# Kernel tuning notes

Measured on AMD Instinct MI355X. Metric: run time of the kernel, lower is better.

## Reference

```python
import jax, jax.numpy as jnp
import numpy as np

B, T, N, DIN, HID, EMB, K, HOR, ODIM = 64, 12, 883, 1, 64, 10, 2, 12, 1


def setup_inputs() -> dict:
    key = jax.random.key(0)
    ks = jax.random.split(key, 12)
    s = 0.1  # keep gate pre-activations sane
    return dict(
        source=jax.random.normal(ks[0], (B, T, N, DIN), jnp.float32),
        node_emb=jax.random.normal(ks[1], (N, EMB), jnp.float32),
        w0_g=jax.random.normal(ks[2], (EMB, K, DIN + HID, 2 * HID), jnp.float32) * s,
        b0_g=jax.random.normal(ks[3], (EMB, 2 * HID), jnp.float32) * s,
        w0_c=jax.random.normal(ks[4], (EMB, K, DIN + HID, HID), jnp.float32) * s,
        b0_c=jax.random.normal(ks[5], (EMB, HID), jnp.float32) * s,
        w1_g=jax.random.normal(ks[6], (EMB, K, 2 * HID, 2 * HID), jnp.float32) * s,
        b1_g=jax.random.normal(ks[7], (EMB, 2 * HID), jnp.float32) * s,
        w1_c=jax.random.normal(ks[8], (EMB, K, 2 * HID, HID), jnp.float32) * s,
        b1_c=jax.random.normal(ks[9], (EMB, HID), jnp.float32) * s,
        conv_w=jax.random.normal(ks[10], (HOR * ODIM, 1, 1, HID), jnp.float32) * s,
        conv_b=jax.random.normal(ks[11], (HOR * ODIM,), jnp.float32) * s,
    )


def _supports(E):
    # adaptive adjacency: softmax(relu(E E^T)) row-wise, Chebyshev set [I, A, ...]
    A = jax.nn.softmax(jax.nn.relu(E @ E.T), axis=1)
    sup = [jnp.eye(E.shape[0], dtype=A.dtype), A]
    for _ in range(2, K):
        sup.append(2.0 * (A @ sup[-1]) - sup[-2])
    return jnp.stack(sup)  # [K, N, N]


def _gconv(x, E, sup, wpool, bpool):
    # x: [B,N,Cin] -> [B,N,Cout]; node-specific weights pooled from embeddings
    w = jnp.einsum('nd,dkio->nkio', E, wpool)          # [N,K,Cin,Cout]
    b = E @ bpool                                      # [N,Cout]
    xg = jnp.einsum('knm,bmc->bnkc', sup, x)           # [B,N,K,Cin]
    return jnp.einsum('bnki,nkio->bno', xg, w) + b


def _cell(x, h, E, sup, wg, bg, wc, bc):
    zr = jax.nn.sigmoid(_gconv(jnp.concatenate([x, h], -1), E, sup, wg, bg))
    z, r = jnp.split(zr, 2, axis=-1)
    hc = jnp.tanh(_gconv(jnp.concatenate([x, z * h], -1), E, sup, wc, bc))
    return r * h + (1.0 - r) * hc


def reference(source, node_emb, w0_g, b0_g, w0_c, b0_c, w1_g, b1_g, w1_c, b1_c, conv_w, conv_b):
    sup = _supports(node_emb)
    cur = jnp.transpose(source, (1, 0, 2, 3))  # [T,B,N,C]
    for wg, bg, wc, bc in ((w0_g, b0_g, w0_c, b0_c), (w1_g, b1_g, w1_c, b1_c)):
        h0 = jnp.zeros((source.shape[0], N, HID), source.dtype)

        def step(h, xt, wg=wg, bg=bg, wc=wc, bc=bc):
            hn = _cell(xt, h, node_emb, sup, wg, bg, wc, bc)
            return hn, hn

        _, cur = jax.lax.scan(step, h0, cur)  # [T,B,N,HID]
    last = cur[-1]  # [B,N,HID]
    # Conv2d(1, HOR*ODIM, kernel=(1,HID)) over [B,1,N,HID] == contraction over HID
    out = jnp.einsum('bnh,oh->bon', last, conv_w[:, 0, 0, :]) + conv_b[None, :, None]
    out = out.reshape(-1, HOR, ODIM, N).transpose(0, 1, 3, 2)  # [B,HOR,N,ODIM]
    return out
```

## Files before the change

### kernel.cpp

```cpp
#include <hip/hip_runtime.h>
#include <cstddef>

#define NN 883
#define BB 64
#define TT 12
#define EMB 10
#define KPAD 896

typedef short short8 __attribute__((ext_vector_type(8)));
typedef _Float16 half8 __attribute__((ext_vector_type(8)));
typedef float f32x4 __attribute__((ext_vector_type(4)));

__device__ __forceinline__ void split_f16(float v, _Float16* hp, _Float16* lp) {
  _Float16 h = (_Float16)v;
  *hp = h;
  *lp = (_Float16)(v - (float)h);
}

__global__ __launch_bounds__(256) void adj_kernel(const float* __restrict__ E,
                                                  _Float16* __restrict__ Ah,
                                                  _Float16* __restrict__ Al) {
  const int n = blockIdx.x;
  const int tid = threadIdx.x;
  __shared__ float sE[EMB];
  __shared__ float sred[256];
  if (tid < EMB) sE[tid] = E[n * EMB + tid];
  __syncthreads();
  float d[4];
  float lmax = 0.0f;
#pragma unroll
  for (int q = 0; q < 4; ++q) {
    int m = tid + q * 256;
    d[q] = 0.0f;
    if (m < NN) {
      float s = 0.0f;
#pragma unroll
      for (int e = 0; e < EMB; ++e) s += sE[e] * E[m * EMB + e];
      d[q] = fmaxf(s, 0.0f);
      lmax = fmaxf(lmax, d[q]);
    }
  }
  sred[tid] = lmax;
  __syncthreads();
  for (int s = 128; s > 0; s >>= 1) {
    if (tid < s) sred[tid] = fmaxf(sred[tid], sred[tid + s]);
    __syncthreads();
  }
  const float mx = sred[0];
  __syncthreads();
  float lsum = 0.0f;
#pragma unroll
  for (int q = 0; q < 4; ++q) {
    int m = tid + q * 256;
    if (m < NN) {
      d[q] = expf(d[q] - mx);
      lsum += d[q];
    }
  }
  sred[tid] = lsum;
  __syncthreads();
  for (int s = 128; s > 0; s >>= 1) {
    if (tid < s) sred[tid] += sred[tid + s];
    __syncthreads();
  }
  const float inv = 1.0f / sred[0];
#pragma unroll
  for (int q = 0; q < 4; ++q) {
    int m = tid + q * 256;
    if (m < KPAD) {
      float v = (m < NN) ? d[q] * inv : 0.0f;
      split_f16(v, &Ah[(size_t)n * KPAD + m], &Al[(size_t)n * KPAD + m]);
    }
  }
}

__global__ __launch_bounds__(256) void mfma_gemm3(const _Float16* __restrict__ Ah,
                                                  const _Float16* __restrict__ Al,
                                                  const _Float16* __restrict__ Xh,
                                                  const _Float16* __restrict__ Xl,
                                                  _Float16* __restrict__ Gh,
                                                  _Float16* __restrict__ Gl, int L) {
  __shared__ _Float16 sA[2][128][40];
  __shared__ _Float16 sX[2][4][128][8];
  const int tid = threadIdx.x;
  const int lane = tid & 63;
  const int wid = tid >> 6;
  const int wm = (wid >> 1) * 64, wn = (wid & 1) * 64;
  const int bm = blockIdx.y * 128;
  const int bl = blockIdx.x * 128;
  const int l15 = lane & 15, l4 = lane >> 4;

  f32x4 acc[4][4] = {};

  const int xlp = (tid & 63) * 2;
  const int xko = tid >> 6;

  for (int k0 = 0; k0 < KPAD; k0 += 32) {
    __syncthreads();
#pragma unroll
    for (int p = 0; p < 2; ++p) {
      int i = tid + p * 256;
      int m = i >> 2, k8 = (i & 3) * 8;
      *(half8*)&sA[0][m][k8] = *(const half8*)&Ah[(size_t)(bm + m) * KPAD + k0 + k8];
      *(half8*)&sA[1][m][k8] = *(const half8*)&Al[(size_t)(bm + m) * KPAD + k0 + k8];
    }
    {
      int gl = bl + xlp;
      int kb = k0 + xko * 8;
#pragma unroll
      for (int buf = 0; buf < 2; ++buf) {
        const _Float16* Xp = buf ? Xl : Xh;
        unsigned int v[8];
#pragma unroll
        for (int j = 0; j < 8; ++j)
          v[j] = *(const unsigned int*)&Xp[(size_t)(kb + j) * L + gl];
        short8 lo, hi;
#pragma unroll
        for (int j = 0; j < 8; ++j) {
          lo[j] = (short)(v[j] & 0xFFFFu);
          hi[j] = (short)(v[j] >> 16);
        }
        *(short8*)&sX[buf][xko][xlp][0] = lo;
        *(short8*)&sX[buf][xko][xlp + 1][0] = hi;
      }
    }
    __syncthreads();
    half8 afh[4], afl[4], bfh[4], bfl[4];
#pragma unroll
    for (int mi = 0; mi < 4; ++mi) {
      afh[mi] = *(half8*)&sA[0][wm + mi * 16 + l15][l4 * 8];
      afl[mi] = *(half8*)&sA[1][wm + mi * 16 + l15][l4 * 8];
    }
#pragma unroll
    for (int ni = 0; ni < 4; ++ni) {
      bfh[ni] = *(half8*)&sX[0][l4][wn + ni * 16 + l15][0];
      bfl[ni] = *(half8*)&sX[1][l4][wn + ni * 16 + l15][0];
    }
#pragma unroll
    for (int mi = 0; mi < 4; ++mi)
#pragma unroll
      for (int ni = 0; ni < 4; ++ni) {
        acc[mi][ni] = __builtin_amdgcn_mfma_f32_16x16x32_f16(afh[mi], bfh[ni],
                                                             acc[mi][ni], 0, 0, 0);
        acc[mi][ni] = __builtin_amdgcn_mfma_f32_16x16x32_f16(afh[mi], bfl[ni],
                                                             acc[mi][ni], 0, 0, 0);
        acc[mi][ni] = __builtin_amdgcn_mfma_f32_16x16x32_f16(afl[mi], bfh[ni],
                                                             acc[mi][ni], 0, 0, 0);
      }
  }
#pragma unroll
  for (int mi = 0; mi < 4; ++mi) {
    int row0 = bm + wm + mi * 16 + l4 * 4;
#pragma unroll
    for (int ni = 0; ni < 4; ++ni) {
      int col = bl + wn + ni * 16 + l15;
#pragma unroll
      for (int r = 0; r < 4; ++r) {
        int row = row0 + r;
        if (row < NN)
          split_f16(acc[mi][ni][r], &Gh[(size_t)row * L + col],
                    &Gl[(size_t)row * L + col]);
      }
    }
  }
}

__global__ __launch_bounds__(256) void srcall_kernel(const float* __restrict__ src,
                                                     _Float16* __restrict__ Xsh,
                                                     _Float16* __restrict__ Xsl) {
  int i = blockIdx.x * 256 + threadIdx.x;
  if (i >= NN * BB * TT) return;
  int t = i % TT;
  int nb = i / TT;
  int b = nb & 63, n = nb >> 6;
  float v = src[((size_t)b * TT + t) * NN + n];
  size_t idx = (size_t)n * (TT * 512) + (size_t)t * 512 + (size_t)b * 8;
  split_f16(v, &Xsh[idx], &Xsl[idx]);
}

template <int CS, int CIN, int XSPLIT, int OW, int COUT>
__global__ __launch_bounds__(256) void wgen_pre(const float* __restrict__ E,
                                                const float* __restrict__ wpool,
                                                _Float16* __restrict__ Wh,
                                                _Float16* __restrict__ Wl) {
  constexpr int C = COUT / OW;
  constexpr int KD = 2 * CS;
  constexpr int KOW = KD / 8;
  const int bid = blockIdx.x;
  const int n = bid / C;
  const int oc = bid % C;
  if (n >= NN) return;
  const int och = oc * OW;
  const int tid = threadIdx.x;
  __shared__ float sE[EMB];
  if (tid < EMB) sE[tid] = E[n * EMB + tid];
  __syncthreads();
  _Float16* bh = Wh + ((size_t)n * C + oc) * ((size_t)KOW * OW * 8);
  _Float16* bl = Wl + ((size_t)n * C + oc) * ((size_t)KOW * OW * 8);
  const int o = tid & (OW - 1);
  for (int ko = tid / OW; ko < KOW; ko += 256 / OW) {
    half8 hv, lv;
#pragma unroll
    for (int j = 0; j < 8; ++j) {
      const int k = ko * 8 + j;
      const int kk = (k >= CS) ? 1 : 0;
      const int kc = k - kk * CS;
      int ii;
      if (CS == CIN) ii = kc;
      else ii = (kc == 0) ? 0 : ((kc >= XSPLIT) ? kc - XSPLIT + 1 : -1);
      float w = 0.0f;
      if (ii >= 0) {
        const float* wp = wpool + ((size_t)kk * CIN + ii) * COUT + och + o;
#pragma unroll
        for (int d = 0; d < EMB; ++d)
          w += sE[d] * wp[(size_t)d * (2 * CIN * COUT)];
      }
      _Float16 hh = (_Float16)w;
      hv[j] = hh;
      lv[j] = (_Float16)(w - (float)hh);
    }
    *(half8*)&bh[((size_t)ko * OW + o) * 8] = hv;
    *(half8*)&bl[((size_t)ko * OW + o) * 8] = lv;
  }
}

template <int CS, int CIN, int XSPLIT, int OW, bool GATE>
__global__ __launch_bounds__(256) void gconv_fused(
    const _Float16* __restrict__ IXh, const _Float16* __restrict__ IXl, int sIX, int oIX,
    const _Float16* __restrict__ IZh, const _Float16* __restrict__ IZl, int sIZ, int oIZ,
    const _Float16* __restrict__ DXh, const _Float16* __restrict__ DXl, int sDX, int oDX,
    const _Float16* __restrict__ DZh, const _Float16* __restrict__ DZl, int sDZ, int oDZ,
    const float* __restrict__ E, const float* __restrict__ wpool,
    const float* __restrict__ bpool, const float* __restrict__ ZRin,
    const _Float16* __restrict__ Hh, const _Float16* __restrict__ Hl, int hb,
    float* __restrict__ ZRout,
    _Float16* __restrict__ XAh, _Float16* __restrict__ XAl, int csA, int cbA,
    const _Float16* __restrict__ PWh, const _Float16* __restrict__ PWl) {
  constexpr int COUT = GATE ? 128 : 64;
  constexpr int C = COUT / OW;
  constexpr int KD = 2 * CS;
  constexpr int KP = (KD + 31) & ~31;
  constexpr int KOW = KD / 8;
  const int bid = blockIdx.x;
  const int xcd = bid & 7;
  const int rest = bid >> 3;
  const int oc = rest % C;
  const int pq = rest / C;
  const int p = pq * 8 + xcd;
  const int nA = p * 2;
  if (nA >= NN) return;
  const int och = oc * OW;
  const int tid = threadIdx.x;
  const int lane = tid & 63, wid = tid >> 6;
  const int ns = wid >> 1;
  const int wm = (wid & 1) * 32;
  const int l15 = lane & 15, l4 = lane >> 4;
  const int myn = nA + ns;
  const int anode = (myn < NN) ? myn : nA;

  __shared__ float sE[2][EMB];
  __shared__ float sB[2][OW];
  __shared__ _Float16 sWh[2][KOW * OW * 8];
  __shared__ _Float16 sWl[2][KOW * OW * 8];

  if (tid < 2 * EMB) {
    const int s = tid / EMB, d = tid - s * EMB;
    const int node = nA + s;
    sE[s][d] = (node < NN) ? E[node * EMB + d] : 0.0f;
  }
  __syncthreads();

  if (PWh != nullptr) {
    for (int i = tid; i < 2 * KOW * OW; i += 256) {
      const int s = i / (KOW * OW);
      const int r = i - s * (KOW * OW);
      const int node = nA + s;
      half8 hv = (half8)(_Float16)0.f, lv = (half8)(_Float16)0.f;
      if (node < NN) {
        const size_t wb =
            ((size_t)node * C + oc) * ((size_t)KOW * OW * 8) + (size_t)r * 8;
        hv = *(const half8*)&PWh[wb];
        lv = *(const half8*)&PWl[wb];
      }
      *(half8*)&sWh[s][(size_t)r * 8] = hv;
      *(half8*)&sWl[s][(size_t)r * 8] = lv;
    }
  } else {
    const int o = tid & (OW - 1);
    for (int ko = tid / OW; ko < KOW; ko += 256 / OW) {
      half8 hv0, lv0, hv1, lv1;
#pragma unroll
      for (int j = 0; j < 8; ++j) {
        const int k = ko * 8 + j;
        const int kk = (k >= CS) ? 1 : 0;
        const int kc = k - kk * CS;
        int ii;
        if (CS == CIN) ii = kc;
        else ii = (kc == 0) ? 0 : ((kc >= XSPLIT) ? kc - XSPLIT + 1 : -1);
        float w0 = 0.0f, w1 = 0.0f;
        if (ii >= 0) {
          const float* wp = wpool + ((size_t)kk * CIN + ii) * COUT + och + o;
#pragma unroll
          for (int d = 0; d < EMB; ++d) {
            const float wv = wp[(size_t)d * (2 * CIN * COUT)];
            w0 += sE[0][d] * wv;
            w1 += sE[1][d] * wv;
          }
        }
        _Float16 h0 = (_Float16)w0;
        hv0[j] = h0;
        lv0[j] = (_Float16)(w0 - (float)h0);
        _Float16 h1 = (_Float16)w1;
        hv1[j] = h1;
        lv1[j] = (_Float16)(w1 - (float)h1);
      }
      *(half8*)&sWh[0][((size_t)ko * OW + o) * 8] = hv0;
      *(half8*)&sWl[0][((size_t)ko * OW + o) * 8] = lv0;
      *(half8*)&sWh[1][((size_t)ko * OW + o) * 8] = hv1;
      *(half8*)&sWl[1][((size_t)ko * OW + o) * 8] = lv1;
    }
  }
  if (tid < 2 * OW) {
    const int s = tid / OW, o = tid - s * OW;
    float bb = 0.0f;
#pragma unroll
    for (int d = 0; d < EMB; ++d) bb += sE[s][d] * bpool[d * COUT + och + o];
    sB[s][o] = bb;
  }
  __syncthreads();

  const size_t bIX = (size_t)anode * sIX + (size_t)oIX * 512;
  const size_t bIZ = (size_t)anode * sIZ + (size_t)oIZ * 512;
  const size_t bDX = (size_t)anode * sDX + (size_t)oDX * 512;
  const size_t bDZ = (size_t)anode * sDZ + (size_t)oDZ * 512;
  f32x4 acc[2][2] = {};
  for (int k0 = 0; k0 < KP; k0 += 32) {
    const int kq = k0 + l4 * 8;
    half8 ah[2], al[2];
#pragma unroll
    for (int mt = 0; mt < 2; ++mt) {
      const int b = wm + mt * 16 + l15;
      if (kq < XSPLIT) {
        const size_t o = bIX + (size_t)(kq >> 3) * 512 + (size_t)b * 8;
        ah[mt] = *(const half8*)&IXh[o];
        al[mt] = *(const half8*)&IXl[o];
      } else if (kq < CS) {
        const size_t o = bIZ + (size_t)((kq - XSPLIT) >> 3) * 512 + (size_t)b * 8;
        ah[mt] = *(const half8*)&IZh[o];
        al[mt] = *(const half8*)&IZl[o];
      } else if (kq < CS + XSPLIT) {
        const size_t o = bDX + (size_t)((kq - CS) >> 3) * 512 + (size_t)b * 8;
        ah[mt] = *(const half8*)&DXh[o];
        al[mt] = *(const half8*)&DXl[o];
      } else if (kq < KD) {
        const size_t o =
            bDZ + (size_t)((kq - CS - XSPLIT) >> 3) * 512 + (size_t)b * 8;
        ah[mt] = *(const half8*)&DZh[o];
        al[mt] = *(const half8*)&DZl[o];
      } else {
        ah[mt] = (half8)(_Float16)0.f;
        al[mt] = (half8)(_Float16)0.f;
      }
    }
    const int koi = kq >> 3;
    half8 bh[2], bl[2];
#pragma unroll
    for (int nt = 0; nt < 2; ++nt) {
      const int ol = nt * 16 + l15;
      if (KP == KD || kq < KD) {
        bh[nt] = *(const half8*)&sWh[ns][((size_t)koi * OW + ol) * 8];
        bl[nt] = *(const half8*)&sWl[ns][((size_t)koi * OW + ol) * 8];
      } else {
        bh[nt] = (half8)(_Float16)0.f;
        bl[nt] = (half8)(_Float16)0.f;
      }
    }
#pragma unroll
    for (int mt = 0; mt < 2; ++mt)
#pragma unroll
      for (int nt = 0; nt < 2; ++nt) {
        acc[mt][nt] =
            __builtin_amdgcn_mfma_f32_16x16x32_f16(ah[mt], bh[nt], acc[mt][nt], 0, 0, 0);
        acc[mt][nt] =
            __builtin_amdgcn_mfma_f32_16x16x32_f16(ah[mt], bl[nt], acc[mt][nt], 0, 0, 0);
        acc[mt][nt] =
            __builtin_amdgcn_mfma_f32_16x16x32_f16(al[mt], bh[nt], acc[mt][nt], 0, 0, 0);
      }
  }

  if (myn < NN) {
#pragma unroll
    for (int mt = 0; mt < 2; ++mt) {
#pragma unroll
      for (int nt = 0; nt < 2; ++nt) {
        const int ol = nt * 16 + l15;
        const int og = och + ol;
        const float bias = sB[ns][ol];
#pragma unroll
        for (int r = 0; r < 4; ++r) {
          const int b = wm + mt * 16 + l4 * 4 + r;
          const size_t nb = (size_t)myn * 64 + b;
          const float v = acc[mt][nt][r] + bias;
          if constexpr (GATE) {
            const float s = 1.0f / (1.0f + expf(-v));
            if (og < 64) {
              const int ch = hb + og;
              const size_t ih = (size_t)myn * 8192 + (size_t)(ch >> 3) * 512 +
                                (size_t)b * 8 + (ch & 7);
              const float hold = (float)Hh[ih] + (float)Hl[ih];
              const float zh = s * hold;
              const int c2 = cbA + og;
              size_t ia = (size_t)myn * 64 * csA + (size_t)(c2 >> 3) * 512 +
                          (size_t)b * 8 + (c2 & 7);
              split_f16(zh, &XAh[ia], &XAl[ia]);
            } else {
              ZRout[nb * 64 + (og - 64)] = s;
            }
          } else {
            const float hc = tanhf(v);
            const float rr = ZRin[nb * 64 + og];
            const int cA = cbA + og;
            const size_t ia = (size_t)myn * 64 * csA + (size_t)(cA >> 3) * 512 +
                              (size_t)b * 8 + (cA & 7);
            const float hold = (float)XAh[ia] + (float)XAl[ia];
            const float hn = rr * hold + (1.0f - rr) * hc;
            split_f16(hn, &XAh[ia], &XAl[ia]);
          }
        }
      }
    }
  }
}

__global__ __launch_bounds__(256) void head_kernel(const _Float16* __restrict__ Hh,
                                                   const _Float16* __restrict__ Hl,
                                                   const float* __restrict__ cw,
                                                   const float* __restrict__ cb,
                                                   float* __restrict__ out) {
  int i = blockIdx.x * 256 + threadIdx.x;
  if (i >= BB * NN) return;
  int n = i % NN, b = i / NN;
  float hv[64];
#pragma unroll
  for (int j = 0; j < 64; ++j) {
    const int c = 64 + j;
    const size_t ia =
        (size_t)n * 8192 + (size_t)(c >> 3) * 512 + (size_t)b * 8 + (c & 7);
    hv[j] = (float)Hh[ia] + (float)Hl[ia];
  }
  for (int o = 0; o < 12; ++o) {
    float s = cb[o];
#pragma unroll
    for (int j = 0; j < 64; ++j) s += hv[j] * cw[o * 64 + j];
    out[((size_t)b * 12 + o) * NN + n] = s;
  }
}

__global__ __launch_bounds__(256) void zero_u16(unsigned short* __restrict__ p,
                                                size_t count) {
  size_t i = (size_t)blockIdx.x * 256 + threadIdx.x;
  if (i < count) p[i] = 0;
}

extern "C" void kernel_launch(void* const* d_in, const int* in_sizes, int n_in,
                              void* d_out, int out_size, void* d_ws, size_t ws_size,
                              hipStream_t stream) {
  const float* src = (const float*)d_in[0];
  const float* E = (const float*)d_in[1];
  const float* w0g = (const float*)d_in[2];
  const float* b0g = (const float*)d_in[3];
  const float* w0c = (const float*)d_in[4];
  const float* b0c = (const float*)d_in[5];
  const float* w1g = (const float*)d_in[6];
  const float* b1g = (const float*)d_in[7];
  const float* w1c = (const float*)d_in[8];
  const float* b1c = (const float*)d_in[9];
  const float* cw = (const float*)d_in[10];
  const float* cb = (const float*)d_in[11];
  float* out = (float*)d_out;
  float* ws = (float*)d_ws;

  size_t off = 0;
  auto alloc = [&](size_t cnt) {
    float* p = ws + off;
    off += (cnt + 63) & ~(size_t)63;
    return p;
  };
  const int LS = TT * 512;
  const int L1 = 64 * 128;
  const int LZ = 64 * 64;
  _Float16* Ah = (_Float16*)alloc((size_t)KPAD * KPAD / 2);
  _Float16* Al = (_Float16*)alloc((size_t)KPAD * KPAD / 2);
  _Float16* Xsh = (_Float16*)alloc((size_t)KPAD * LS / 2);
  _Float16* Xsl = (_Float16*)alloc((size_t)KPAD * LS / 2);
  _Float16* Gxh = (_Float16*)alloc((size_t)KPAD * LS / 2);
  _Float16* Gxl = (_Float16*)alloc((size_t)KPAD * LS / 2);
  _Float16* X1ah = (_Float16*)alloc((size_t)KPAD * L1 / 2);
  _Float16* X1al = (_Float16*)alloc((size_t)KPAD * L1 / 2);
  _Float16* Xzh = (_Float16*)alloc((size_t)KPAD * LZ / 2);
  _Float16* Xzl = (_Float16*)alloc((size_t)KPAD * LZ / 2);
  _Float16* Gl1h = (_Float16*)alloc((size_t)KPAD * L1 / 2);
  _Float16* Gl1l = (_Float16*)alloc((size_t)KPAD * L1 / 2);
  _Float16* Gzh = (_Float16*)alloc((size_t)KPAD * LZ / 2);
  _Float16* Gzl = (_Float16*)alloc((size_t)KPAD * LZ / 2);
  float* ZR = alloc((size_t)NN * BB * 64);
  if (off * sizeof(float) > ws_size) return;

  const size_t wsfl = ws_size / sizeof(float);
  const size_t whalves[4] = {(size_t)NN * 18432, (size_t)NN * 9216,
                             (size_t)NN * 32768, (size_t)NN * 16384};
  const size_t avail = (wsfl > off) ? (wsfl - off) : 0;
  int best = 0;
  size_t bestsz = 0;
  for (int s = 1; s < 16; ++s) {
    size_t tot = 0;
    for (int f = 0; f < 4; ++f)
      if (s & (1 << f)) tot += whalves[f] + 128;
    if (tot <= avail && tot > bestsz) {
      bestsz = tot;
      best = s;
    }
  }
  _Float16 *W0gh = nullptr, *W0gl = nullptr, *W0ch = nullptr, *W0cl = nullptr;
  _Float16 *W1gh = nullptr, *W1gl = nullptr, *W1ch = nullptr, *W1cl = nullptr;
  if (best & 1) {
    W0gh = (_Float16*)alloc(whalves[0] / 2);
    W0gl = (_Float16*)alloc(whalves[0] / 2);
  }
  if (best & 2) {
    W0ch = (_Float16*)alloc(whalves[1] / 2);
    W0cl = (_Float16*)alloc(whalves[1] / 2);
  }
  if (best & 4) {
    W1gh = (_Float16*)alloc(whalves[2] / 2);
    W1gl = (_Float16*)alloc(whalves[2] / 2);
  }
  if (best & 8) {
    W1ch = (_Float16*)alloc(whalves[3] / 2);
    W1cl = (_Float16*)alloc(whalves[3] / 2);
  }

  adj_kernel<<<NN, 256, 0, stream>>>(E, Ah, Al);
  {
    size_t cx = (size_t)2 * KPAD * (LS + LS + L1 + LZ + L1 + LZ);
    zero_u16<<<(int)((cx + 255) / 256), 256, 0, stream>>>((unsigned short*)Xsh, cx);
  }
  srcall_kernel<<<(NN * BB * TT + 255) / 256, 256, 0, stream>>>(src, Xsh, Xsl);
  mfma_gemm3<<<dim3(LS / 128, 7), 256, 0, stream>>>(Ah, Al, Xsh, Xsl, Gxh, Gxl, LS);
  if (W0gh) wgen_pre<72, 65, 8, 32, 128><<<NN * 4, 256, 0, stream>>>(E, w0g, W0gh, W0gl);
  if (W0ch) wgen_pre<72, 65, 8, 32, 64><<<NN * 2, 256, 0, stream>>>(E, w0c, W0ch, W0cl);
  if (W1gh) wgen_pre<128, 128, 64, 32, 128><<<NN * 4, 256, 0, stream>>>(E, w1g, W1gh, W1gl);
  if (W1ch) wgen_pre<128, 128, 64, 32, 64><<<NN * 2, 256, 0, stream>>>(E, w1c, W1ch, W1cl);

  const int gx1 = L1 / 128;
  const int gxz = LZ / 128;
  const int PQ = (((NN + 1) / 2 + 7) / 8) * 8;
  const int g_gate = PQ * 4;
  const int g_cand = PQ * 2;
  for (int t = 0; t < TT; ++t) {
    gconv_fused<72, 65, 8, 32, true><<<g_gate, 256, 0, stream>>>(
        Xsh, Xsl, LS, t, X1ah, X1al, L1, 0, Gxh, Gxl, LS, t, Gl1h, Gl1l, L1, 0,
        E, w0g, b0g, nullptr, X1ah, X1al, 0, ZR, Xzh, Xzl, 64, 0, W0gh, W0gl);
    mfma_gemm3<<<dim3(gxz, 7), 256, 0, stream>>>(Ah, Al, Xzh, Xzl, Gzh, Gzl, LZ);
    gconv_fused<72, 65, 8, 32, false><<<g_cand, 256, 0, stream>>>(
        Xsh, Xsl, LS, t, Xzh, Xzl, LZ, 0, Gxh, Gxl, LS, t, Gzh, Gzl, LZ, 0,
        E, w0c, b0c, ZR, nullptr, nullptr, 0, nullptr, X1ah, X1al, 128, 0, W0ch, W0cl);
    mfma_gemm3<<<dim3(gx1, 7), 256, 0, stream>>>(Ah, Al, X1ah, X1al, Gl1h, Gl1l, L1);
    gconv_fused<128, 128, 64, 32, true><<<g_gate, 256, 0, stream>>>(
        X1ah, X1al, L1, 0, X1ah, X1al, L1, 8, Gl1h, Gl1l, L1, 0, Gl1h, Gl1l, L1, 8,
        E, w1g, b1g, nullptr, X1ah, X1al, 64, ZR, Xzh, Xzl, 64, 0, W1gh, W1gl);
    mfma_gemm3<<<dim3(gxz, 7), 256, 0, stream>>>(Ah, Al, Xzh, Xzl, Gzh, Gzl, LZ);
    gconv_fused<128, 128, 64, 32, false><<<g_cand, 256, 0, stream>>>(
        X1ah, X1al, L1, 0, Xzh, Xzl, LZ, 0, Gl1h, Gl1l, L1, 0, Gzh, Gzl, LZ, 0,
        E, w1c, b1c, ZR, nullptr, nullptr, 0, nullptr, X1ah, X1al, 128, 64, W1ch, W1cl);
  }
  head_kernel<<<(BB * NN + 255) / 256, 256, 0, stream>>>(X1ah, X1al, cw, cb, out);
}
```

Baseline: 3.782 ms.

## Read precomputed weights directly from global memory and shrink zero-init

When node-specific weights are precomputed, gconv_fused gains a compile-time PRE variant. It reads the MFMA B operands straight from global memory instead of first staging them through shared memory. That drops a shared-memory copy pass and a barrier per block and cuts LDS use, which may raise occupancy. The cost is repeated global/L2 reads inside the K loop. Separately, the source scatter now writes full 8-half vectors and the zero-init only clears the padded regions, using vectorized stores.

```diff
diff --git a/kernel.cpp b/kernel.cpp
--- a/kernel.cpp
+++ b/kernel.cpp
@@ -170,12 +170,18 @@
                                                      _Float16* __restrict__ Xsl) {
   int i = blockIdx.x * 256 + threadIdx.x;
   if (i >= NN * BB * TT) return;
-  int t = i % TT;
-  int nb = i / TT;
-  int b = nb & 63, n = nb >> 6;
+  int b = i & 63;
+  int rest = i >> 6;
+  int t = rest % TT;
+  int n = rest / TT;
   float v = src[((size_t)b * TT + t) * NN + n];
   size_t idx = (size_t)n * (TT * 512) + (size_t)t * 512 + (size_t)b * 8;
-  split_f16(v, &Xsh[idx], &Xsl[idx]);
+  half8 hv = (half8)(_Float16)0.f, lv = (half8)(_Float16)0.f;
+  _Float16 hh = (_Float16)v;
+  hv[0] = hh;
+  lv[0] = (_Float16)(v - (float)hh);
+  *(half8*)&Xsh[idx] = hv;
+  *(half8*)&Xsl[idx] = lv;
 }
 
 template <int CS, int CIN, int XSPLIT, int OW, int COUT>
@@ -224,7 +230,7 @@
   }
 }
 
-template <int CS, int CIN, int XSPLIT, int OW, bool GATE>
+template <int CS, int CIN, int XSPLIT, int OW, bool GATE, bool PRE>
 __global__ __launch_bounds__(256) void gconv_fused(
     const _Float16* __restrict__ IXh, const _Float16* __restrict__ IXl, int sIX, int oIX,
     const _Float16* __restrict__ IZh, const _Float16* __restrict__ IZl, int sIZ, int oIZ,
@@ -260,8 +266,8 @@
 
   __shared__ float sE[2][EMB];
   __shared__ float sB[2][OW];
-  __shared__ _Float16 sWh[2][KOW * OW * 8];
-  __shared__ _Float16 sWl[2][KOW * OW * 8];
+  __shared__ _Float16 sWh[PRE ? 8 : 2 * KOW * OW * 8];
+  __shared__ _Float16 sWl[PRE ? 8 : 2 * KOW * OW * 8];
 
   if (tid < 2 * EMB) {
     const int s = tid / EMB, d = tid - s * EMB;
@@ -270,22 +276,7 @@
   }
   __syncthreads();
 
-  if (PWh != nullptr) {
-    for (int i = tid; i < 2 * KOW * OW; i += 256) {
-      const int s = i / (KOW * OW);
-      const int r = i - s * (KOW * OW);
-      const int node = nA + s;
-      half8 hv = (half8)(_Float16)0.f, lv = (half8)(_Float16)0.f;
-      if (node < NN) {
-        const size_t wb =
-            ((size_t)node * C + oc) * ((size_t)KOW * OW * 8) + (size_t)r * 8;
-        hv = *(const half8*)&PWh[wb];
-        lv = *(const half8*)&PWl[wb];
-      }
-      *(half8*)&sWh[s][(size_t)r * 8] = hv;
-      *(half8*)&sWl[s][(size_t)r * 8] = lv;
-    }
-  } else {
+  if constexpr (!PRE) {
     const int o = tid & (OW - 1);
     for (int ko = tid / OW; ko < KOW; ko += 256 / OW) {
       half8 hv0, lv0, hv1, lv1;
@@ -314,10 +305,10 @@
         hv1[j] = h1;
         lv1[j] = (_Float16)(w1 - (float)h1);
       }
-      *(half8*)&sWh[0][((size_t)ko * OW + o) * 8] = hv0;
-      *(half8*)&sWl[0][((size_t)ko * OW + o) * 8] = lv0;
-      *(half8*)&sWh[1][((size_t)ko * OW + o) * 8] = hv1;
-      *(half8*)&sWl[1][((size_t)ko * OW + o) * 8] = lv1;
+      *(half8*)&sWh[((size_t)ko * OW + o) * 8] = hv0;
+      *(half8*)&sWl[((size_t)ko * OW + o) * 8] = lv0;
+      *(half8*)&sWh[(size_t)KOW * OW * 8 + ((size_t)ko * OW + o) * 8] = hv1;
+      *(half8*)&sWl[(size_t)KOW * OW * 8 + ((size_t)ko * OW + o) * 8] = lv1;
     }
   }
   if (tid < 2 * OW) {
@@ -333,6 +324,8 @@
   const size_t bIZ = (size_t)anode * sIZ + (size_t)oIZ * 512;
   const size_t bDX = (size_t)anode * sDX + (size_t)oDX * 512;
   const size_t bDZ = (size_t)anode * sDZ + (size_t)oDZ * 512;
+  const size_t wtile = (size_t)KOW * OW * 8;
+  const size_t wbase = PRE ? ((size_t)anode * C + oc) * wtile : (size_t)ns * wtile;
   f32x4 acc[2][2] = {};
   for (int k0 = 0; k0 < KP; k0 += 32) {
     const int kq = k0 + l4 * 8;
@@ -368,8 +361,14 @@
     for (int nt = 0; nt < 2; ++nt) {
       const int ol = nt * 16 + l15;
       if (KP == KD || kq < KD) {
-        bh[nt] = *(const half8*)&sWh[ns][((size_t)koi * OW + ol) * 8];
-        bl[nt] = *(const half8*)&sWl[ns][((size_t)koi * OW + ol) * 8];
+        const size_t wo = wbase + ((size_t)koi * OW + ol) * 8;
+        if constexpr (PRE) {
+          bh[nt] = *(const half8*)&PWh[wo];
+          bl[nt] = *(const half8*)&PWl[wo];
+        } else {
+          bh[nt] = *(const half8*)&sWh[wo];
+          bl[nt] = *(const half8*)&sWl[wo];
+        }
       } else {
         bh[nt] = (half8)(_Float16)0.f;
         bl[nt] = (half8)(_Float16)0.f;
@@ -456,10 +455,10 @@
   }
 }
 
-__global__ __launch_bounds__(256) void zero_u16(unsigned short* __restrict__ p,
-                                                size_t count) {
+__global__ __launch_bounds__(256) void zero_h8(_Float16* __restrict__ p,
+                                               size_t cnt8) {
   size_t i = (size_t)blockIdx.x * 256 + threadIdx.x;
-  if (i < count) p[i] = 0;
+  if (i < cnt8) *(half8*)&p[i * 8] = (half8)(_Float16)0.f;
 }
 
 extern "C" void kernel_launch(void* const* d_in, const int* in_sizes, int n_in,
@@ -542,8 +541,13 @@
 
   adj_kernel<<<NN, 256, 0, stream>>>(E, Ah, Al);
   {
-    size_t cx = (size_t)2 * KPAD * (LS + LS + L1 + LZ + L1 + LZ);
-    zero_u16<<<(int)((cx + 255) / 256), 256, 0, stream>>>((unsigned short*)Xsh, cx);
+    size_t cbig8 = (size_t)2 * KPAD * (L1 + LZ + L1) / 8;
+    zero_h8<<<(int)((cbig8 + 255) / 256), 256, 0, stream>>>(X1ah, cbig8);
+    size_t cpad8 = (size_t)(KPAD - NN) * LS / 8;
+    zero_h8<<<(int)((cpad8 + 255) / 256), 256, 0, stream>>>(
+        Xsh + (size_t)NN * LS, cpad8);
+    zero_h8<<<(int)((cpad8 + 255) / 256), 256, 0, stream>>>(
+        Xsl + (size_t)NN * LS, cpad8);
   }
   srcall_kernel<<<(NN * BB * TT + 255) / 256, 256, 0, stream>>>(src, Xsh, Xsl);
   mfma_gemm3<<<dim3(LS / 128, 7), 256, 0, stream>>>(Ah, Al, Xsh, Xsl, Gxh, Gxl, LS);
@@ -558,21 +562,41 @@
   const int g_gate = PQ * 4;
   const int g_cand = PQ * 2;
   for (int t = 0; t < TT; ++t) {
-    gconv_fused<72, 65, 8, 32, true><<<g_gate, 256, 0, stream>>>(
-        Xsh, Xsl, LS, t, X1ah, X1al, L1, 0, Gxh, Gxl, LS, t, Gl1h, Gl1l, L1, 0,
-        E, w0g, b0g, nullptr, X1ah, X1al, 0, ZR, Xzh, Xzl, 64, 0, W0gh, W0gl);
+    if (W0gh)
+      gconv_fused<72, 65, 8, 32, true, true><<<g_gate, 256, 0, stream>>>(
+          Xsh, Xsl, LS, t, X1ah, X1al, L1, 0, Gxh, Gxl, LS, t, Gl1h, Gl1l, L1, 0,
+          E, w0g, b0g, nullptr, X1ah, X1al, 0, ZR, Xzh, Xzl, 64, 0, W0gh, W0gl);
+    else
+      gconv_fused<72, 65, 8, 32, true, false><<<g_gate, 256, 0, stream>>>(
+          Xsh, Xsl, LS, t, X1ah, X1al, L1, 0, Gxh, Gxl, LS, t, Gl1h, Gl1l, L1, 0,
+          E, w0g, b0g, nullptr, X1ah, X1al, 0, ZR, Xzh, Xzl, 64, 0, nullptr, nullptr);
     mfma_gemm3<<<dim3(gxz, 7), 256, 0, stream>>>(Ah, Al, Xzh, Xzl, Gzh, Gzl, LZ);
-    gconv_fused<72, 65, 8, 32, false><<<g_cand, 256, 0, stream>>>(
-        Xsh, Xsl, LS, t, Xzh, Xzl, LZ, 0, Gxh, Gxl, LS, t, Gzh, Gzl, LZ, 0,
-        E, w0c, b0c, ZR, nullptr, nullptr, 0, nullptr, X1ah, X1al, 128, 0, W0ch, W0cl);
+    if (W0ch)
+      gconv_fused<72, 65, 8, 32, false, true><<<g_cand, 256, 0, stream>>>(
+          Xsh, Xsl, LS, t, Xzh, Xzl, LZ, 0, Gxh, Gxl, LS, t, Gzh, Gzl, LZ, 0,
+          E, w0c, b0c, ZR, nullptr, nullptr, 0, nullptr, X1ah, X1al, 128, 0, W0ch, W0cl);
+    else
+      gconv_fused<72, 65, 8, 32, false, false><<<g_cand, 256, 0, stream>>>(
+          Xsh, Xsl, LS, t, Xzh, Xzl, LZ, 0, Gxh, Gxl, LS, t, Gzh, Gzl, LZ, 0,
+          E, w0c, b0c, ZR, nullptr, nullptr, 0, nullptr, X1ah, X1al, 128, 0, nullptr, nullptr);
     mfma_gemm3<<<dim3(gx1, 7), 256, 0, stream>>>(Ah, Al, X1ah, X1al, Gl1h, Gl1l, L1);
-    gconv_fused<128, 128, 64, 32, true><<<g_gate, 256, 0, stream>>>(
-        X1ah, X1al, L1, 0, X1ah, X1al, L1, 8, Gl1h, Gl1l, L1, 0, Gl1h, Gl1l, L1, 8,
-        E, w1g, b1g, nullptr, X1ah, X1al, 64, ZR, Xzh, Xzl, 64, 0, W1gh, W1gl);
+    if (W1gh)
+      gconv_fused<128, 128, 64, 32, true, true><<<g_gate, 256, 0, stream>>>(
+          X1ah, X1al, L1, 0, X1ah, X1al, L1, 8, Gl1h, Gl1l, L1, 0, Gl1h, Gl1l, L1, 8,
+          E, w1g, b1g, nullptr, X1ah, X1al, 64, ZR, Xzh, Xzl, 64, 0, W1gh, W1gl);
+    else
+      gconv_fused<128, 128, 64, 32, true, false><<<g_gate, 256, 0, stream>>>(
+          X1ah, X1al, L1, 0, X1ah, X1al, L1, 8, Gl1h, Gl1l, L1, 0, Gl1h, Gl1l, L1, 8,
+          E, w1g, b1g, nullptr, X1ah, X1al, 64, ZR, Xzh, Xzl, 64, 0, nullptr, nullptr);
     mfma_gemm3<<<dim3(gxz, 7), 256, 0, stream>>>(Ah, Al, Xzh, Xzl, Gzh, Gzl, LZ);
-    gconv_fused<128, 128, 64, 32, false><<<g_cand, 256, 0, stream>>>(
-        X1ah, X1al, L1, 0, Xzh, Xzl, LZ, 0, Gl1h, Gl1l, L1, 0, Gzh, Gzl, LZ, 0,
-        E, w1c, b1c, ZR, nullptr, nullptr, 0, nullptr, X1ah, X1al, 128, 64, W1ch, W1cl);
+    if (W1ch)
+      gconv_fused<128, 128, 64, 32, false, true><<<g_cand, 256, 0, stream>>>(
+          X1ah, X1al, L1, 0, Xzh, Xzl, LZ, 0, Gl1h, Gl1l, L1, 0, Gzh, Gzl, LZ, 0,
+          E, w1c, b1c, ZR, nullptr, nullptr, 0, nullptr, X1ah, X1al, 128, 64, W1ch, W1cl);
+    else
+      gconv_fused<128, 128, 64, 32, false, false><<<g_cand, 256, 0, stream>>>(
+          X1ah, X1al, L1, 0, Xzh, Xzl, LZ, 0, Gl1h, Gl1l, L1, 0, Gzh, Gzl, LZ, 0,
+          E, w1c, b1c, ZR, nullptr, nullptr, 0, nullptr, X1ah, X1al, 128, 64, nullptr, nullptr);
   }
   head_kernel<<<(BB * NN + 255) / 256, 256, 0, stream>>>(X1ah, X1al, cw, cb, out);
 }
```

Measured after the change: 3.555 ms. 1.06x faster.
